# Kernel tuning notes

Measured on AMD Instinct MI355X. Metric: run time of the kernel, lower is better.

## Reference

```python
import jax, jax.numpy as jnp
import numpy as np
import math

FACTOR = 5

def setup_inputs() -> dict:
    key = jax.random.key(0)
    k1, k2, k3, k4 = jax.random.split(key, 4)
    B, L, H, D = 2, 4096, 8, 64
    sample_k = min(FACTOR * int(np.ceil(np.log(L))), L)  # 45
    return {
        "queries": jax.random.normal(k1, (B, L, H, D), dtype=jnp.float32),
        "keys": jax.random.normal(k2, (B, L, H, D), dtype=jnp.float32),
        "values": jax.random.normal(k3, (B, L, H, D), dtype=jnp.float32),
        "attn_mask": jnp.zeros((1,), dtype=bool),  # unused (mask_flag=False)
        "index_sample": jax.random.randint(k4, (L, sample_k), 0, L, dtype=jnp.int64),
    }

def reference(queries, keys, values, attn_mask, index_sample):
    B, L_Q, H, D = queries.shape
    L_K = keys.shape[1]
    # [B,L,H,D] -> [B,H,L,D]
    q = jnp.transpose(queries, (0, 2, 1, 3))
    k = jnp.transpose(keys, (0, 2, 1, 3))
    v = jnp.transpose(values, (0, 2, 1, 3))

    n_top = min(FACTOR * int(np.ceil(np.log(L_Q))), L_Q)  # u

    # --- _prob_QK ---
    # K_sample[b,h,l,s,e] = k[b,h,index_sample[l,s],e]
    K_sample = k[:, :, index_sample, :]                      # [B,H,L_Q,S,E]
    Q_K_sample = jnp.einsum('bhle,bhlse->bhls', q, K_sample)  # [B,H,L_Q,S]
    # sparsity measure: max - mean(over full L_K as in torch code)
    M = Q_K_sample.max(axis=-1) - Q_K_sample.sum(axis=-1) / L_K  # [B,H,L_Q]
    M_top = jax.lax.top_k(M, n_top)[1]                        # [B,H,u] indices

    Q_reduce = jnp.take_along_axis(q, M_top[..., None], axis=2)  # [B,H,u,E]
    scores_top = jnp.einsum('bhue,bhke->bhuk', Q_reduce, k)      # [B,H,u,L_K]

    scale = 1.0 / math.sqrt(D)
    attn = jax.nn.softmax(scale * scores_top, axis=-1)           # [B,H,u,L_K]
    context_in_q = jnp.einsum('bhuk,bhkd->bhud', attn, v)        # [B,H,u,D]

    # scatter selected contexts into zero-initialized tensor
    b_idx = jnp.arange(B)[:, None, None]
    h_idx = jnp.arange(H)[None, :, None]
    context = jnp.zeros((B, H, L_Q, D), dtype=queries.dtype)
    context = context.at[b_idx, h_idx, M_top].set(context_in_q)

    return jnp.transpose(context, (0, 2, 1, 3))  # [B,L_Q,H,D]
```

## Files before the change

### kernel.cpp

```cpp
#include <hip/hip_runtime.h>
#include <math.h>

#define B_ 2
#define L_ 4096
#define H_ 8
#define D_ 64
#define S_ 45
#define NTOP_ 45
#define SCALE 0.125f
#define TKEYS 64
#define NSPLIT 64

template<int CTRL>
__device__ __forceinline__ float dpp_permf(float x) {
    return __int_as_float(__builtin_amdgcn_update_dpp(
        0, __float_as_int(x), CTRL, 0xF, 0xF, true));
}

__global__ __launch_bounds__(256) void compute_M_kernel(
    const float* __restrict__ q, const float* __restrict__ k,
    const int* __restrict__ samp, float* __restrict__ M) {
    __shared__ int sIdx[8 * 48];
    int tid = threadIdx.x;
    int g   = blockIdx.x;
    int xcd = g & 7;
    int chunk = g >> 3;
    int b  = xcd >> 2;
    int h0 = (xcd & 3) * 2;
    int l0 = chunk * 8;

    for (int i = tid; i < 8 * S_; i += 256) {
        int qq = i / S_, ss = i - qq * S_;
        sIdx[qq * 48 + ss] = samp[(long)(l0 + qq) * S_ + ss];
    }
    if (tid < 24) sIdx[(tid / 3) * 48 + S_ + (tid % 3)] = 0;
    __syncthreads();

    int lane = tid & 63, wave = tid >> 6;
    int c  = lane & 31;
    int q8 = wave * 2 + (lane >> 5);
    int l  = l0 + q8;

    float4 q4 = ((const float4*)(q + (((long)(b * L_ + l)) * H_ + h0) * D_))[c];
    const float4* kb4 = (const float4*)(k + ((long)b * L_ * H_ + h0) * (long)D_);
    const int* myIdx = sIdx + q8 * 48;

    float4 f0 = kb4[(long)myIdx[0] * 128 + c];
    float4 f1 = kb4[(long)myIdx[1] * 128 + c];
    float4 f2 = kb4[(long)myIdx[2] * 128 + c];

    float vmax = -INFINITY, vsum = 0.f;
    #pragma unroll 3
    for (int s = 0; s < S_; ++s) {
        float4 nf = kb4[(long)myIdx[s + 3] * 128 + c];
        float p = q4.x * f0.x + q4.y * f0.y + q4.z * f0.z + q4.w * f0.w;
        p += dpp_permf<0xB1>(p);
        p += dpp_permf<0x4E>(p);
        p += __shfl_xor(p, 4, 64);
        p += __shfl_xor(p, 8, 64);
        vmax = fmaxf(vmax, p);
        vsum += p;
        f0 = f1; f1 = f2; f2 = nf;
    }
    if ((lane & 15) == 0) {
        int h = h0 + ((lane >> 4) & 1);
        M[(long)(b * 8 + h) * L_ + l] = vmax - vsum * (1.0f / (float)L_);
    }
}

__global__ __launch_bounds__(256) void topk_kernel(
    const float* __restrict__ M, int* __restrict__ topIdx) {
    __shared__ unsigned int hist[256];
    __shared__ unsigned int suf[257];
    __shared__ unsigned int wsum[4];
    __shared__ int sBin, sRemain, sCnt, sTieCnt;
    __shared__ int tie[64];

    int bh = blockIdx.x, tid = threadIdx.x;
    int lane = tid & 63, wave = tid >> 6;
    const float* row = M + (long)bh * L_;

    unsigned int key[16];
    #pragma unroll
    for (int j = 0; j < 16; ++j) {
        unsigned int bts = __float_as_uint(row[tid + 256 * j]);
        key[j] = bts ^ ((unsigned int)((int)bts >> 31) | 0x80000000u);
    }

    unsigned int prefix = 0, pmask = 0;
    int remain = NTOP_;
    #pragma unroll 1
    for (int pass = 3; pass >= 0; --pass) {
        int shift = pass * 8;
        hist[tid] = 0;
        __syncthreads();
        #pragma unroll
        for (int j = 0; j < 16; ++j) {
            if ((key[j] & pmask) == prefix)
                atomicAdd(&hist[(key[j] >> shift) & 255u], 1u);
        }
        __syncthreads();
        unsigned int s = hist[tid];
        #pragma unroll
        for (int off = 1; off < 64; off <<= 1) {
            unsigned int o = __shfl_down(s, off, 64);
            if (lane + off < 64) s += o;
        }
        if (lane == 0) wsum[wave] = s;
        __syncthreads();
        unsigned int add = 0;
        for (int w = wave + 1; w < 4; ++w) add += wsum[w];
        s += add;
        suf[tid] = s;
        if (tid == 0) suf[256] = 0;
        __syncthreads();
        if (suf[tid] >= (unsigned int)remain && suf[tid + 1] < (unsigned int)remain) {
            sBin = tid;
            sRemain = remain - (int)suf[tid + 1];
        }
        __syncthreads();
        prefix |= ((unsigned int)sBin) << shift;
        pmask  |= 0xFFu << shift;
        remain  = sRemain;
        __syncthreads();
    }

    if (tid == 0) { sCnt = 0; sTieCnt = 0; }
    __syncthreads();
    int* outRow = topIdx + bh * NTOP_;
    #pragma unroll
    for (int j = 0; j < 16; ++j) {
        int idx = tid + 256 * j;
        if (key[j] > prefix) {
            int pos = atomicAdd(&sCnt, 1);
            outRow[pos] = idx;
        } else if (key[j] == prefix) {
            int tp = atomicAdd(&sTieCnt, 1);
            if (tp < 64) tie[tp] = idx;
        }
    }
    __syncthreads();
    if (tid == 0) {
        int base = sCnt;
        int tc = sTieCnt < 64 ? sTieCnt : 64;
        for (int t = 0; t < remain; ++t) {
            int mi = 0x7fffffff, mj = 0;
            for (int j2 = 0; j2 < tc; ++j2)
                if (tie[j2] < mi) { mi = tie[j2]; mj = j2; }
            outRow[base + t] = mi;
            tie[mj] = 0x7fffffff;
        }
    }
}

#define STRIDE 68
__global__ __launch_bounds__(256, 2) void attn_strip_kernel(
    const float* __restrict__ q, const float* __restrict__ k,
    const float* __restrict__ v, const int* __restrict__ topIdx,
    float* __restrict__ pOut, float* __restrict__ plPart,
    float* __restrict__ out, int nsplit) {
    __shared__ float sQ[48 * STRIDE];
    __shared__ float sK[TKEYS * STRIDE];
    __shared__ float sV[TKEYS * STRIDE];
    __shared__ float sP[48 * STRIDE];

    int g = blockIdx.x;
    int xcd = g & 7;
    int s0 = g >> 3;
    int grp = s0 / nsplit;
    int bh = xcd + 8 * grp;
    int split = s0 - grp * nsplit;
    int b = bh >> 3, h = bh & 7;
    int tid = threadIdx.x;
    int key0 = split * TKEYS;

    #pragma unroll
    for (int j = 0; j < 3; ++j) {
        int i = tid + 256 * j;
        int u = i >> 4, d4 = i & 15;
        float4 val = make_float4(0.f, 0.f, 0.f, 0.f);
        if (u < NTOP_) {
            int lq = topIdx[bh * NTOP_ + u];
            val = *(const float4*)(q + (((long)(b * L_ + lq)) * H_ + h) * D_ + 4 * d4);
        }
        *(float4*)(sQ + u * STRIDE + 4 * d4) = val;
    }
    #pragma unroll
    for (int j = 0; j < 4; ++j) {
        int i = tid + 256 * j;
        int r = i >> 4, d4 = i & 15;
        long off = (((long)(b * L_ + key0 + r)) * H_ + h) * D_ + 4 * d4;
        *(float4*)(sK + r * STRIDE + 4 * d4) = *(const float4*)(k + off);
        *(float4*)(sV + r * STRIDE + 4 * d4) = *(const float4*)(v + off);
    }

    {
        long total4 = (long)B_ * L_ * H_ * D_ / 4;
        long per = total4 / ((long)nsplit * 16);
        float4* ob = (float4*)out + (long)g * per;
        float4 z = make_float4(0.f, 0.f, 0.f, 0.f);
        for (long j = tid; j < per; j += 256) ob[j] = z;
    }
    __syncthreads();

    int tx = tid & 15, ty = tid >> 4;
    float acc[3][4];
    #pragma unroll
    for (int i = 0; i < 3; ++i)
        #pragma unroll
        for (int j = 0; j < 4; ++j) acc[i][j] = 0.f;

    #pragma unroll 4
    for (int d4 = 0; d4 < 16; ++d4) {
        float4 qv[3];
        #pragma unroll
        for (int i = 0; i < 3; ++i)
            qv[i] = *(const float4*)(sQ + (3 * ty + i) * STRIDE + 4 * d4);
        #pragma unroll
        for (int j = 0; j < 4; ++j) {
            float4 kv = *(const float4*)(sK + (tx + 16 * j) * STRIDE + 4 * d4);
            #pragma unroll
            for (int i = 0; i < 3; ++i)
                acc[i][j] += qv[i].x * kv.x + qv[i].y * kv.y + qv[i].z * kv.z + qv[i].w * kv.w;
        }
    }
    #pragma unroll
    for (int i = 0; i < 3; ++i) {
        #pragma unroll
        for (int j = 0; j < 4; ++j)
            sP[(3 * ty + i) * STRIDE + tx + 16 * j] = __expf(acc[i][j] * SCALE);
    }
    __syncthreads();

    int dx = tid & 15, uy = tid >> 4;
    float o[3][4];
    float ls[3];
    #pragma unroll
    for (int i = 0; i < 3; ++i) {
        ls[i] = 0.f;
        #pragma unroll
        for (int c = 0; c < 4; ++c) o[i][c] = 0.f;
    }
    #pragma unroll 4
    for (int k4 = 0; k4 < 16; ++k4) {
        float pa[3][4];
        #pragma unroll
        for (int i = 0; i < 3; ++i)
            *(float4*)pa[i] = *(const float4*)(sP + (3 * uy + i) * STRIDE + 4 * k4);
        #pragma unroll
        for (int c = 0; c < 4; ++c) {
            float4 vr = *(const float4*)(sV + (4 * k4 + c) * STRIDE + 4 * dx);
            #pragma unroll
            for (int i = 0; i < 3; ++i) {
                o[i][0] += pa[i][c] * vr.x;
                o[i][1] += pa[i][c] * vr.y;
                o[i][2] += pa[i][c] * vr.z;
                o[i][3] += pa[i][c] * vr.w;
                ls[i]   += pa[i][c];
            }
        }
    }
    #pragma unroll
    for (int i = 0; i < 3; ++i) {
        int u = 3 * uy + i;
        if (u < NTOP_) {
            long base = ((long)(split * 16 + bh) * NTOP_ + u) * D_;
            *(float4*)(pOut + base + 4 * dx) = make_float4(o[i][0], o[i][1], o[i][2], o[i][3]);
            if (dx == 0) plPart[(long)(split * 16 + bh) * NTOP_ + u] = ls[i];
        }
    }
}

__global__ __launch_bounds__(256) void reduce_norm_kernel(
    const int* __restrict__ topIdx, const float* __restrict__ pOut,
    const float* __restrict__ plPart, float* __restrict__ out, int nsplit) {
    __shared__ float part[4][64];
    __shared__ float lpart[4];
    int u = blockIdx.x, bh = blockIdx.y;
    int b = bh >> 3, h = bh & 7;
    int tid = threadIdx.x;
    int d = tid & 63, sg = tid >> 6;
    float acc = 0.f, lsum = 0.f;
    for (int s = sg; s < nsplit; s += 4) {
        acc  += pOut[((long)(s * 16 + bh) * NTOP_ + u) * D_ + d];
        lsum += plPart[(long)(s * 16 + bh) * NTOP_ + u];
    }
    part[sg][d] = acc;
    if (d == 0) lpart[sg] = lsum;
    __syncthreads();
    if (sg == 0) {
        float a = part[0][d] + part[1][d] + part[2][d] + part[3][d];
        float lt = lpart[0] + lpart[1] + lpart[2] + lpart[3];
        int lq = topIdx[bh * NTOP_ + u];
        out[(((long)(b * L_ + lq)) * H_ + h) * D_ + d] = a / lt;
    }
}

extern "C" void kernel_launch(void* const* d_in, const int* in_sizes, int n_in,
                              void* d_out, int out_size, void* d_ws, size_t ws_size,
                              hipStream_t stream) {
    const float* q = (const float*)d_in[0];
    const float* k = (const float*)d_in[1];
    const float* v = (const float*)d_in[2];
    const int* samp = (const int*)d_in[4];
    float* out = (float*)d_out;

    char* ws = (char*)d_ws;
    const size_t mBytes   = (size_t)B_ * H_ * L_ * sizeof(float);
    const size_t topBytes = (size_t)B_ * H_ * NTOP_ * sizeof(int);
    const size_t plBytes  = (size_t)NSPLIT * 16 * NTOP_ * sizeof(float);
    float* M      = (float*)ws;
    int*   topIdx = (int*)(ws + mBytes);
    float* plPart = (float*)(ws + mBytes + topBytes);
    float* pOut   = (float*)(ws + mBytes + topBytes + plBytes);

    int nsplit = NSPLIT;
    while (nsplit > 1) {
        size_t need = mBytes + topBytes + plBytes +
                      (size_t)nsplit * 16 * NTOP_ * D_ * sizeof(float);
        if (need <= ws_size) break;
        nsplit >>= 1;
    }

    compute_M_kernel<<<4096, 256, 0, stream>>>(q, k, samp, M);

    topk_kernel<<<B_ * H_, 256, 0, stream>>>(M, topIdx);

    attn_strip_kernel<<<nsplit * B_ * H_, 256, 0, stream>>>(
        q, k, v, topIdx, pOut, plPart, out, nsplit);

    dim3 gn(NTOP_, B_ * H_);
    reduce_norm_kernel<<<gn, 256, 0, stream>>>(topIdx, pOut, plPart, out, nsplit);
}
```

Before: 155.3 us.

## Fuse split reduction into attention kernel via last-block atomic counter

Removes the separate reduce_norm kernel launch. Each attention block bumps a per-(b,h) atomic counter, and the last block to finish sums the partial outputs and denominators across splits and scatters the normalized rows. Zeroing of the output now covers the block's own (b,h) rows, so it cannot race with that final scatter. sP now reuses sQ's shared memory to allow 3 blocks per CU. The cost is a serialized tail: one block per (b,h) reduces all splits alone, which adds latency.

```diff
diff --git a/kernel.cpp b/kernel.cpp
--- a/kernel.cpp
+++ b/kernel.cpp
@@ -69,7 +69,7 @@
 }
 
 __global__ __launch_bounds__(256) void topk_kernel(
-    const float* __restrict__ M, int* __restrict__ topIdx) {
+    const float* __restrict__ M, int* __restrict__ topIdx, int* __restrict__ cnt) {
     __shared__ unsigned int hist[256];
     __shared__ unsigned int suf[257];
     __shared__ unsigned int wsum[4];
@@ -79,6 +79,8 @@
     int bh = blockIdx.x, tid = threadIdx.x;
     int lane = tid & 63, wave = tid >> 6;
     const float* row = M + (long)bh * L_;
+
+    if (tid == 0) cnt[bh] = 0;
 
     unsigned int key[16];
     #pragma unroll
@@ -154,15 +156,16 @@
 }
 
 #define STRIDE 68
-__global__ __launch_bounds__(256, 2) void attn_strip_kernel(
+__global__ __launch_bounds__(256, 3) void attn_strip_kernel(
     const float* __restrict__ q, const float* __restrict__ k,
     const float* __restrict__ v, const int* __restrict__ topIdx,
     float* __restrict__ pOut, float* __restrict__ plPart,
-    float* __restrict__ out, int nsplit) {
+    float* __restrict__ out, int* __restrict__ cnt, int nsplit) {
     __shared__ float sQ[48 * STRIDE];
     __shared__ float sK[TKEYS * STRIDE];
     __shared__ float sV[TKEYS * STRIDE];
-    __shared__ float sP[48 * STRIDE];
+    __shared__ float lsumS[NTOP_];
+    __shared__ int isLastS;
 
     int g = blockIdx.x;
     int xcd = g & 7;
@@ -195,11 +198,13 @@
     }
 
     {
-        long total4 = (long)B_ * L_ * H_ * D_ / 4;
-        long per = total4 / ((long)nsplit * 16);
-        float4* ob = (float4*)out + (long)g * per;
+        int rows = L_ / nsplit;
+        int row0 = split * rows;
         float4 z = make_float4(0.f, 0.f, 0.f, 0.f);
-        for (long j = tid; j < per; j += 256) ob[j] = z;
+        for (int idx = tid; idx < rows * 16; idx += 256) {
+            int r = idx >> 4, c4 = idx & 15;
+            *((float4*)(out + (((long)(b * L_ + row0 + r)) * H_ + h) * D_) + c4) = z;
+        }
     }
     __syncthreads();
 
@@ -224,6 +229,9 @@
                 acc[i][j] += qv[i].x * kv.x + qv[i].y * kv.y + qv[i].z * kv.z + qv[i].w * kv.w;
         }
     }
+    __syncthreads();
+
+    float* sP = sQ;
     #pragma unroll
     for (int i = 0; i < 3; ++i) {
         #pragma unroll
@@ -269,30 +277,30 @@
             if (dx == 0) plPart[(long)(split * 16 + bh) * NTOP_ + u] = ls[i];
         }
     }
-}
-
-__global__ __launch_bounds__(256) void reduce_norm_kernel(
-    const int* __restrict__ topIdx, const float* __restrict__ pOut,
-    const float* __restrict__ plPart, float* __restrict__ out, int nsplit) {
-    __shared__ float part[4][64];
-    __shared__ float lpart[4];
-    int u = blockIdx.x, bh = blockIdx.y;
-    int b = bh >> 3, h = bh & 7;
-    int tid = threadIdx.x;
-    int d = tid & 63, sg = tid >> 6;
-    float acc = 0.f, lsum = 0.f;
-    for (int s = sg; s < nsplit; s += 4) {
-        acc  += pOut[((long)(s * 16 + bh) * NTOP_ + u) * D_ + d];
-        lsum += plPart[(long)(s * 16 + bh) * NTOP_ + u];
-    }
-    part[sg][d] = acc;
-    if (d == 0) lpart[sg] = lsum;
-    __syncthreads();
-    if (sg == 0) {
-        float a = part[0][d] + part[1][d] + part[2][d] + part[3][d];
-        float lt = lpart[0] + lpart[1] + lpart[2] + lpart[3];
-        int lq = topIdx[bh * NTOP_ + u];
-        out[(((long)(b * L_ + lq)) * H_ + h) * D_ + d] = a / lt;
+
+    __threadfence();
+    if (tid == 0) {
+        int old = atomicAdd(&cnt[bh], 1);
+        isLastS = (old == nsplit - 1) ? 1 : 0;
+    }
+    __syncthreads();
+    if (isLastS) {
+        for (int u = tid; u < NTOP_; u += 256) {
+            float lt = 0.f;
+            for (int s = 0; s < nsplit; ++s)
+                lt += plPart[(long)(s * 16 + bh) * NTOP_ + u];
+            lsumS[u] = lt;
+        }
+        __syncthreads();
+        for (int idx = tid; idx < NTOP_ * D_; idx += 256) {
+            int u = idx >> 6, d = idx & 63;
+            float a = 0.f;
+            const float* pb = pOut + ((long)bh * NTOP_ + u) * D_ + d;
+            #pragma unroll 8
+            for (int s = 0; s < nsplit; ++s) a += pb[(long)s * 16 * NTOP_ * D_];
+            int lq = topIdx[bh * NTOP_ + u];
+            out[(((long)(b * L_ + lq)) * H_ + h) * D_ + d] = a / lsumS[u];
+        }
     }
 }
 
@@ -309,14 +317,16 @@
     const size_t mBytes   = (size_t)B_ * H_ * L_ * sizeof(float);
     const size_t topBytes = (size_t)B_ * H_ * NTOP_ * sizeof(int);
     const size_t plBytes  = (size_t)NSPLIT * 16 * NTOP_ * sizeof(float);
+    const size_t cntBytes = 256;
     float* M      = (float*)ws;
     int*   topIdx = (int*)(ws + mBytes);
     float* plPart = (float*)(ws + mBytes + topBytes);
-    float* pOut   = (float*)(ws + mBytes + topBytes + plBytes);
+    int*   cnt    = (int*)(ws + mBytes + topBytes + plBytes);
+    float* pOut   = (float*)(ws + mBytes + topBytes + plBytes + cntBytes);
 
     int nsplit = NSPLIT;
     while (nsplit > 1) {
-        size_t need = mBytes + topBytes + plBytes +
+        size_t need = mBytes + topBytes + plBytes + cntBytes +
                       (size_t)nsplit * 16 * NTOP_ * D_ * sizeof(float);
         if (need <= ws_size) break;
         nsplit >>= 1;
@@ -324,11 +334,8 @@
 
     compute_M_kernel<<<4096, 256, 0, stream>>>(q, k, samp, M);
 
-    topk_kernel<<<B_ * H_, 256, 0, stream>>>(M, topIdx);
+    topk_kernel<<<B_ * H_, 256, 0, stream>>>(M, topIdx, cnt);
 
     attn_strip_kernel<<<nsplit * B_ * H_, 256, 0, stream>>>(
-        q, k, v, topIdx, pOut, plPart, out, nsplit);
-
-    dim3 gn(NTOP_, B_ * H_);
-    reduce_norm_kernel<<<gn, 256, 0, stream>>>(topIdx, pOut, plPart, out, nsplit);
-}
+        q, k, v, topIdx, pOut, plPart, out, cnt, nsplit);
+}
```

Result: slower. 322.3 us (+107.5%).
